# Kernel optimization log

Measured on AMD Instinct MI355X. Metric: run time of the kernel, lower is better.

Reference implementation:

```python
import jax, jax.numpy as jnp
import numpy as np

B, C, N, O, K = 4, 64, 8192, 128, 20


def setup_inputs() -> dict:
    key = jax.random.key(0)
    k1, k2, k3 = jax.random.split(key, 3)
    x = jax.random.normal(k1, (B, C, N), dtype=jnp.float32)
    # Conv2d(2C, 2C, 1, bias=False) weight squeezed to [2C, 2C]
    W1 = jax.random.normal(k2, (2 * C, 2 * C), dtype=jnp.float32) * (1.0 / np.sqrt(2 * C))
    # Conv2d(2C, O, 1, bias=False) weight squeezed to [O, 2C]
    W2 = jax.random.normal(k3, (O, 2 * C), dtype=jnp.float32) * (1.0 / np.sqrt(2 * C))
    return {"x": x, "W1": W1, "W2": W2, "spiral_size": K}


def _knn_idx(x, k):
    # x: [B, C, N]; negative squared pairwise distance, top-k = k nearest (incl. self)
    inner = -2.0 * jnp.einsum('bcn,bcm->bnm', x, x)          # [B, N, N]
    xx = jnp.sum(x * x, axis=1)                               # [B, N]
    pd = -xx[:, :, None] - inner - xx[:, None, :]             # [B, N, N]
    return jax.lax.top_k(pd, k)[1]                            # [B, N, k] int32


def reference(x, W1, W2, spiral_size):
    b, c, n = x.shape
    idx = _knn_idx(x, spiral_size)                            # [B, N, K]
    xt = jnp.transpose(x, (0, 2, 1))                          # [B, N, C]
    spirals = xt[jnp.arange(b)[:, None, None], idx]           # [B, N, K, C] neighbor gather
    center = jnp.broadcast_to(xt[:, :, None, :], spirals.shape)
    feats = jnp.concatenate([spirals - center, center], axis=-1)  # [B, N, K, 2C]
    h = jnp.einsum('bnkc,dc->bnkd', feats, W1)                # 1x1 conv1
    gate = jax.nn.softmax(h, axis=2)                          # softmax over neighbor dim K
    gated = feats * gate                                      # [B, N, K, 2C]
    out = jnp.einsum('bnkc,oc->bon', gated, W2)               # conv2 + sum over K -> [B, O, N]
    return out
```

## Files before the change

kernel.cpp:

```cpp
#include <hip/hip_runtime.h>
#include <math.h>

#define BB 4
#define CC 64
#define NN 8192
#define OO 128
#define KK 20
#define DD 128
#define NT 64
#define BUFSZ 10

typedef short bf16x8 __attribute__((ext_vector_type(8)));
typedef float f32x4 __attribute__((ext_vector_type(4)));
typedef unsigned short u16x8 __attribute__((ext_vector_type(8)));
typedef unsigned long long u64;

typedef __attribute__((address_space(1))) const void gvoid;
typedef __attribute__((address_space(3))) void lvoid;

__device__ __forceinline__ u64 packkey(float v, int idx) {
  unsigned u = __float_as_uint(v);
  unsigned o = ((int)u < 0) ? ~u : (u | 0x80000000u);
  return (((u64)o) << 32) | (unsigned)(~idx);
}
__device__ __forceinline__ float keyval(u64 k) {
  unsigned o = (unsigned)(k >> 32);
  unsigned u = (o & 0x80000000u) ? (o ^ 0x80000000u) : ~o;
  return __uint_as_float(u);
}
#define INITKEY (((u64)0x007FFFFFu) << 32)

__device__ __forceinline__ unsigned short bf_rne(float f) {
  unsigned u = __float_as_uint(f);
  u += 0x7FFFu + ((u >> 16) & 1u);
  return (unsigned short)(u >> 16);
}
__device__ __forceinline__ float bf_f(unsigned short h) {
  return __uint_as_float(((unsigned)h) << 16);
}

__global__ __launch_bounds__(128) void prep_kernel(const float* __restrict__ x,
                                                   float* __restrict__ xx,
                                                   unsigned short* __restrict__ xs) {
  const int tid = threadIdx.x;
  const int b = blockIdx.y;
  const int n0 = blockIdx.x * 128;
  const float* xb = x + (size_t)b * CC * NN;
  float xv[CC];
  float acc = 0.0f;
  #pragma unroll
  for (int c = 0; c < CC; ++c) {
    float v = xb[(size_t)c * NN + n0 + tid];
    acc += v * v;
    xv[c] = v;
  }
  xx[b * NN + n0 + tid] = acc;

  const int n = n0 + tid;
  char* xsrow = ((char*)xs) + ((size_t)b * NN + n) * 384;
  const int swn = (n & 7) << 4;
  #pragma unroll
  for (int gr = 0; gr < 8; ++gr) {
    u16x8 h8, m8, l8;
    #pragma unroll
    for (int e = 0; e < 8; ++e) {
      float v = xv[gr * 8 + e];
      unsigned short h = bf_rne(v);
      float r = v - bf_f(h);
      unsigned short m = bf_rne(r);
      r -= bf_f(m);
      unsigned short l = bf_rne(r);
      h8[e] = (unsigned short)h; m8[e] = m; l8[e] = l;
    }
    *(u16x8*)(xsrow + (((gr * 16) + 0) ^ swn)) = h8;
    *(u16x8*)(xsrow + (((gr * 16) + 128) ^ swn)) = m8;
    *(u16x8*)(xsrow + (((gr * 16) + 256) ^ swn)) = l8;
  }
}

__global__ __launch_bounds__(256, 4) void knn_kernel(
    const unsigned short* __restrict__ xs, const float* __restrict__ xx,
    u64* __restrict__ pkeys) {
  __shared__ __attribute__((aligned(16))) unsigned short atile[64 * 192];
  __shared__ float pdb[4][64][BUFSZ];
  __shared__ unsigned short idb[4][64][BUFSZ];
  __shared__ float cxx[64];
  const int tid = threadIdx.x;
  const int w = tid >> 6;
  const int lane = tid & 63;
  const int r = lane & 15;
  const int g = lane >> 4;
  const int lin = blockIdx.x;
  const int b = (lin & 7) >> 1;
  const int ch = lin & 1;
  const int qg = lin >> 3;
  const int qbase = qg * 64 + w * 16;
  const int q = qbase + r;
  const int cbase = ch * 4096;
  const char* xsb = ((const char*)xs) + (size_t)b * NN * 384;

  bf16x8 bq[3][2];
  {
    const char* qrow = xsb + (size_t)q * 384;
    const int sw = (q & 7) << 4;
    #pragma unroll
    for (int s = 0; s < 3; ++s)
      #pragma unroll
      for (int c = 0; c < 2; ++c)
        bq[s][c] = *(const bf16x8*)(qrow + ((s * 128 + c * 64 + g * 16) ^ sw));
  }
  const float xxq = xx[b * NN + q];

  u64 tk[KK];
  #pragma unroll
  for (int j = 0; j < KK; ++j) tk[j] = INITKEY;
  float minv = -INFINITY;
  int cnt = 0;
  float* pdl = &pdb[w][lane][0];
  unsigned short* idl = &idb[w][lane][0];

  auto stage = [&](int t) {
    const char* src = xsb + (size_t)(cbase + t * 64) * 384;
    char* dst = (char*)atile;
    #pragma unroll
    for (int it = 0; it < 6; ++it) {
      __builtin_amdgcn_global_load_lds(
          (gvoid*)(src + it * 4096 + tid * 16),
          (lvoid*)(dst + it * 4096 + tid * 16), 16, 0, 0);
    }
    if (tid < 16) {
      __builtin_amdgcn_global_load_lds(
          (gvoid*)(xx + b * NN + cbase + t * 64 + tid * 4),
          (lvoid*)(cxx + tid * 4), 16, 0, 0);
    }
  };

  auto rebuild = [&]() {
    int mxc = cnt;
    #pragma unroll
    for (int o = 32; o > 0; o >>= 1) {
      int v = __shfl_xor(mxc, o);
      mxc = mxc > v ? mxc : v;
    }
    for (int i = 0; i < mxc; ++i) {
      u64 k = (i < cnt) ? packkey(pdl[i], (int)idl[i]) : 0ULL;
      if (k > tk[KK - 1]) {
        #pragma unroll
        for (int jj = KK - 1; jj >= 1; --jj)
          tk[jj] = (k > tk[jj - 1]) ? tk[jj - 1] : ((k > tk[jj]) ? k : tk[jj]);
        tk[0] = (k > tk[0]) ? k : tk[0];
      }
    }
    cnt = 0;
    minv = keyval(tk[KK - 1]);
  };

  for (int t = 0; t < NT; ++t) {
    stage(t);
    __syncthreads();

    #pragma unroll
    for (int ct = 0; ct < 4; ++ct) {
      const char* arow = ((const char*)atile) + (ct * 16 + r) * 384;
      const int sw = (r & 7) << 4;
      bf16x8 a6[6];
      #pragma unroll
      for (int c6 = 0; c6 < 6; ++c6)
        a6[c6] = *(const bf16x8*)(arow + ((c6 * 64 + g * 16) ^ sw));
      f32x4 acc = {0.f, 0.f, 0.f, 0.f};
      __builtin_amdgcn_s_setprio(1);
      #pragma unroll
      for (int s = 2; s >= 0; --s)
        #pragma unroll
        for (int c6 = 0; c6 < 6; ++c6)
          acc = __builtin_amdgcn_mfma_f32_16x16x32_bf16(a6[c6], bq[s][c6 & 1],
                                                        acc, 0, 0, 0);
      __builtin_amdgcn_s_setprio(0);
      #pragma unroll
      for (int j = 0; j < 4; ++j) {
        const int ml = ct * 16 + g * 4 + j;
        float pd = (-xxq - (-2.0f * acc[j])) - cxx[ml];
        if (pd > minv) {
          pdl[cnt] = pd;
          idl[cnt] = (unsigned short)(cbase + t * 64 + ml);
          ++cnt;
        }
      }
      if (__any(cnt > 6)) rebuild();
    }
    __syncthreads();
  }

  rebuild();

  for (int pass = 0; pass < 2; ++pass) {
    if (pass) __syncthreads();
    if ((w >> 1) == pass) {
      u64* ml = ((u64*)atile) + (size_t)(w & 1) * 64 * KK;
      #pragma unroll
      for (int j = 0; j < KK; ++j) ml[lane * KK + j] = tk[j];
      if (lane < 16) {
        u64* po = pkeys + (((size_t)b * NN + qbase + lane) * 2 + ch) * KK;
        const u64* L0 = ml + (lane + 0) * KK;
        const u64* L1 = ml + (lane + 16) * KK;
        const u64* L2 = ml + (lane + 32) * KK;
        const u64* L3 = ml + (lane + 48) * KK;
        int p0 = 0, p1 = 0, p2 = 0, p3 = 0;
        u64 h0 = L0[0], h1 = L1[0], h2 = L2[0], h3 = L3[0];
        #pragma unroll
        for (int k = 0; k < KK; ++k) {
          u64 bv = h0; int bc = 0;
          if (h1 > bv) { bv = h1; bc = 1; }
          if (h2 > bv) { bv = h2; bc = 2; }
          if (h3 > bv) { bv = h3; bc = 3; }
          po[k] = bv;
          if (bc == 0)      { ++p0; h0 = (p0 < KK) ? L0[p0] : 0ULL; }
          else if (bc == 1) { ++p1; h1 = (p1 < KK) ? L1[p1] : 0ULL; }
          else if (bc == 2) { ++p2; h2 = (p2 < KK) ? L2[p2] : 0ULL; }
          else              { ++p3; h3 = (p3 < KK) ? L3[p3] : 0ULL; }
        }
      }
    }
  }
}

__global__ __launch_bounds__(256) void merge_kernel(const u64* __restrict__ pkeys,
                                                    int* __restrict__ fidx) {
  const int q = blockIdx.x * 256 + threadIdx.x;
  const u64* pk = pkeys + (size_t)q * 2 * KK;
  int* fo = fidx + (size_t)q * KK;
  int p0 = 0, p1 = 0;
  u64 h0 = pk[0], h1 = pk[KK];
  #pragma unroll
  for (int k = 0; k < KK; ++k) {
    const bool t1 = h1 > h0;
    const u64 bv = t1 ? h1 : h0;
    fo[k] = (int)(~(unsigned)bv);
    if (t1) { ++p1; h1 = (p1 < KK) ? pk[KK + p1] : 0ULL; }
    else    { ++p0; h0 = (p0 < KK) ? pk[p0] : 0ULL; }
  }
}

__global__ __launch_bounds__(256) void w1prep_kernel(const float* __restrict__ W1,
                                                     unsigned short* __restrict__ w1p) {
  for (int e = threadIdx.x; e < 12288; e += 256) {
    const int f = e >> 9;
    const int rr = e & 511;
    const int l = rr >> 3;
    const int j = rr & 7;
    const int pair = f / 3, s = f % 3;
    const int dt = pair >> 1, kc = pair & 1;
    const int d = dt * 16 + (l & 15);
    const int c = kc * 32 + (l >> 4) * 8 + j;
    const float v = W1[d * DD + c];
    const unsigned short h = bf_rne(v);
    float r = v - bf_f(h);
    const unsigned short m = bf_rne(r);
    r -= bf_f(m);
    const unsigned short lo = bf_rne(r);
    w1p[(size_t)f * 512 + l * 8 + j] = (s == 0) ? h : ((s == 1) ? m : lo);
  }
}

#define MFMA16(A, B, C) __builtin_amdgcn_mfma_f32_16x16x32_bf16((A), (B), (C), 0, 0, 0)

template <int SA, int SB>
__device__ __forceinline__ void h_term(const bf16x8 (&a)[3][2][2],
                                       const bf16x8 (&w1f)[24],
                                       f32x4 (&acc)[4][2]) {
  #pragma unroll
  for (int dt = 0; dt < 4; ++dt)
    #pragma unroll
    for (int kc = 0; kc < 2; ++kc) {
      const bf16x8 bf = w1f[(dt * 2 + kc) * 3 + SB];
      acc[dt][0] = MFMA16(a[SA][kc][0], bf, acc[dt][0]);
      acc[dt][1] = MFMA16(a[SA][kc][1], bf, acc[dt][1]);
    }
}

template <int DT>
__device__ __forceinline__ float d1_epi(const bf16x8 (&a)[3][2][2],
                                        bf16x8 id0, bf16x8 id1,
                                        const f32x4 (&acc)[4][2], int g) {
  constexpr int KC = DT >> 1;
  const bf16x8 idp = (DT & 1) ? id1 : id0;
  f32x4 yf0 = {0.f, 0.f, 0.f, 0.f}, yf1 = {0.f, 0.f, 0.f, 0.f};
  yf0 = MFMA16(a[1][KC][0], idp, yf0);
  yf0 = MFMA16(a[0][KC][0], idp, yf0);
  yf1 = MFMA16(a[1][KC][1], idp, yf1);
  yf1 = MFMA16(a[0][KC][1], idp, yf1);
  const f32x4 h0 = acc[DT][0], h1 = acc[DT][1];
  float mx = fmaxf(fmaxf(h0[0], h0[1]), fmaxf(h0[2], h0[3]));
  mx = fmaxf(mx, fmaxf(fmaxf(h1[0], h1[1]), fmaxf(h1[2], h1[3])));
  mx = fmaxf(mx, __shfl_xor(mx, 16));
  mx = fmaxf(mx, __shfl_xor(mx, 32));
  float sl = 0.f, tl = 0.f;
  #pragma unroll
  for (int j = 0; j < 4; ++j) {
    const float e = __expf(h0[j] - mx);
    sl += e; tl += yf0[j] * e;
  }
  if (g == 0) {
    #pragma unroll
    for (int j = 0; j < 4; ++j) {
      const float e = __expf(h1[j] - mx);
      sl += e; tl += yf1[j] * e;
    }
  }
  sl += __shfl_xor(sl, 16); sl += __shfl_xor(sl, 32);
  tl += __shfl_xor(tl, 16); tl += __shfl_xor(tl, 32);
  return tl / sl;
}

__global__ __launch_bounds__(256, 2) void d1_kernel(
    const unsigned short* __restrict__ xs, const int* __restrict__ fidx,
    const unsigned short* __restrict__ w1p, float* __restrict__ gbuf) {
  const int tid = threadIdx.x;
  const int w = tid >> 6;
  const int lane = tid & 63;
  const int r = lane & 15;
  const int g = lane >> 4;
  const int b = blockIdx.y;
  const char* xsb = ((const char*)xs) + (size_t)b * NN * 384;

  bf16x8 w1f[24];
  #pragma unroll
  for (int f = 0; f < 24; ++f)
    w1f[f] = *(const bf16x8*)(((const char*)w1p) + f * 1024 + lane * 16);

  bf16x8 id0, id1;
  #pragma unroll
  for (int j = 0; j < 8; ++j) {
    id0[j] = (g == (r >> 3) && j == (r & 7)) ? (short)0x3F80 : (short)0;
    id1[j] = (g == 2 + (r >> 3) && j == (r & 7)) ? (short)0x3F80 : (short)0;
  }

  for (int i = 0; i < 4; ++i) {
    const int n = blockIdx.x * 16 + w * 4 + i;
    const size_t ng = (size_t)b * NN + n;
    const int* kp = fidx + ng * KK;
    const int row0 = kp[r];
    const int row1 = kp[16 + (r & 3)];
    const char* rp0 = xsb + (size_t)row0 * 384;
    const char* rp1 = xsb + (size_t)row1 * 384;
    const int sw0 = (row0 & 7) << 4, sw1 = (row1 & 7) << 4;

    bf16x8 a[3][2][2];
    #pragma unroll
    for (int s = 0; s < 3; ++s)
      #pragma unroll
      for (int kc = 0; kc < 2; ++kc) {
        const int off = s * 128 + kc * 64 + g * 16;
        a[s][kc][0] = *(const bf16x8*)(rp0 + (off ^ sw0));
        a[s][kc][1] = *(const bf16x8*)(rp1 + (off ^ sw1));
      }

    const char* zrow = xsb + (size_t)n * 384;
    const int swn = (n & 7) << 4;
    float zl;
    {
      const unsigned short zh = *(const unsigned short*)(zrow + ((2 * lane) ^ swn));
      const unsigned short zm = *(const unsigned short*)(zrow + ((128 + 2 * lane) ^ swn));
      const unsigned short zo = *(const unsigned short*)(zrow + ((256 + 2 * lane) ^ swn));
      zl = bf_f(zh) + bf_f(zm) + bf_f(zo);
    }

    f32x4 acc[4][2];
    #pragma unroll
    for (int dt = 0; dt < 4; ++dt) {
      acc[dt][0] = (f32x4){0.f, 0.f, 0.f, 0.f};
      acc[dt][1] = (f32x4){0.f, 0.f, 0.f, 0.f};
    }
    h_term<2, 0>(a, w1f, acc);
    h_term<0, 2>(a, w1f, acc);
    h_term<1, 1>(a, w1f, acc);
    h_term<1, 0>(a, w1f, acc);
    h_term<0, 1>(a, w1f, acc);
    h_term<0, 0>(a, w1f, acc);

    const float t0 = d1_epi<0>(a, id0, id1, acc, g);
    const float t1 = d1_epi<1>(a, id0, id1, acc, g);
    const float t2 = d1_epi<2>(a, id0, id1, acc, g);
    const float t3 = d1_epi<3>(a, id0, id1, acc, g);

    float* go = gbuf + ng * DD;
    go[64 + lane] = zl;
    const float z0 = __shfl(zl, r);
    const float z1 = __shfl(zl, 16 + r);
    const float z2 = __shfl(zl, 32 + r);
    const float z3 = __shfl(zl, 48 + r);
    if (lane < 16) {
      go[r]      = t0 - z0;
      go[16 + r] = t1 - z1;
      go[32 + r] = t2 - z2;
      go[48 + r] = t3 - z3;
    }
  }
}

__global__ __launch_bounds__(256) void d2_kernel(const float* __restrict__ gbuf,
                                                 const float* __restrict__ W2,
                                                 float* __restrict__ out) {
  __shared__ float4 w2s[OO * 32];
  const int tid = threadIdx.x;
  const int b = blockIdx.y;
  const int n0 = blockIdx.x * 32;
  const float4* w2v = (const float4*)W2;
  for (int t = tid; t < OO * 32; t += 256) {
    int o = t >> 5, c4 = t & 31;
    w2s[o * 32 + (c4 ^ (o & 7))] = w2v[t];
  }
  __syncthreads();
  const int og = tid & 7;
  const int ni = tid >> 3;
  const int n = n0 + ni;
  const float4* gp = (const float4*)(gbuf + ((size_t)b * NN + n) * DD);
  float acc[16];
  #pragma unroll
  for (int j = 0; j < 16; ++j) acc[j] = 0.0f;
  for (int c4 = 0; c4 < 32; ++c4) {
    float4 g4 = gp[c4];
    #pragma unroll
    for (int j = 0; j < 16; ++j) {
      const int o = j * 8 + og;
      float4 w4 = w2s[o * 32 + (c4 ^ og)];
      acc[j] += g4.x * w4.x + g4.y * w4.y + g4.z * w4.z + g4.w * w4.w;
    }
  }
  float* outb = out + (size_t)b * OO * NN;
  #pragma unroll
  for (int j = 0; j < 16; ++j) {
    outb[(size_t)(j * 8 + og) * NN + n] = acc[j];
  }
}

extern "C" void kernel_launch(void* const* d_in, const int* in_sizes, int n_in,
                              void* d_out, int out_size, void* d_ws, size_t ws_size,
                              hipStream_t stream) {
  const float* x  = (const float*)d_in[0];
  const float* W1 = (const float*)d_in[1];
  const float* W2 = (const float*)d_in[2];
  float* out = (float*)d_out;
  char* ws = (char*)d_ws;
  unsigned short* xs = (unsigned short*)(ws);
  float* xx = (float*)(ws + 12582912);
  unsigned short* w1p = (unsigned short*)(ws + 12582912);
  int* fidx = (int*)(ws + 12713984);
  u64* pkeys = (u64*)(ws + 15335424);
  float* gbuf = (float*)(ws + 15335424);

  prep_kernel<<<dim3(NN / 128, BB), 128, 0, stream>>>(x, xx, xs);
  knn_kernel<<<dim3(1024), 256, 0, stream>>>(xs, xx, pkeys);
  merge_kernel<<<dim3(BB * NN / 256), 256, 0, stream>>>(pkeys, fidx);
  w1prep_kernel<<<dim3(1), 256, 0, stream>>>(W1, w1p);
  d1_kernel<<<dim3(NN / 16, BB), 256, 0, stream>>>(xs, fidx, w1p, gbuf);
  d2_kernel<<<dim3(NN / 32, BB), 256, 0, stream>>>(gbuf, W2, out);
}
```

Baseline: 708.3 us.

## Halve KNN candidate tile to raise occupancy and add wave-level skip of candidate insertion

Shrinks the per-iteration candidate tile from 64 to 32 points and the per-thread candidate buffer from 10 to 8 entries, which cuts LDS use so the launch bound can ask for 6 blocks per CU instead of 4. The candidate-filter step now computes all four distances first and skips the buffer-insert branch when no lane in the wave beats its current threshold. The merge scratch is split between the tile and buffer memory, since the tile alone is now too small for it. The cost is twice as many barrier and staging iterations, each carrying less MFMA work, and possible register pressure under the tighter launch bound.

```diff
diff --git a/kernel.cpp b/kernel.cpp
--- a/kernel.cpp
+++ b/kernel.cpp
@@ -7,8 +7,11 @@
 #define OO 128
 #define KK 20
 #define DD 128
-#define NT 64
-#define BUFSZ 10
+#define NCH 2
+#define CH (NN / NCH)
+#define TC 32
+#define NT (CH / TC)
+#define BUFSZ 8
 
 typedef short bf16x8 __attribute__((ext_vector_type(8)));
 typedef float f32x4 __attribute__((ext_vector_type(4)));
@@ -78,25 +81,28 @@
   }
 }
 
-__global__ __launch_bounds__(256, 4) void knn_kernel(
+__global__ __launch_bounds__(256, 6) void knn_kernel(
     const unsigned short* __restrict__ xs, const float* __restrict__ xx,
     u64* __restrict__ pkeys) {
-  __shared__ __attribute__((aligned(16))) unsigned short atile[64 * 192];
-  __shared__ float pdb[4][64][BUFSZ];
-  __shared__ unsigned short idb[4][64][BUFSZ];
-  __shared__ float cxx[64];
+  __shared__ __attribute__((aligned(16))) unsigned short atile[TC * 192];
+  __shared__ __attribute__((aligned(16))) char bufmem[4 * 64 * BUFSZ * 6];
+  __shared__ float cxx[TC];
+  float* pdb = (float*)bufmem;
+  unsigned short* idb = (unsigned short*)(bufmem + 4 * 64 * BUFSZ * 4);
+
   const int tid = threadIdx.x;
   const int w = tid >> 6;
   const int lane = tid & 63;
   const int r = lane & 15;
   const int g = lane >> 4;
   const int lin = blockIdx.x;
-  const int b = (lin & 7) >> 1;
-  const int ch = lin & 1;
+  const int xcd = lin & 7;
+  const int b = xcd >> 1;
+  const int ch = xcd & 1;
   const int qg = lin >> 3;
   const int qbase = qg * 64 + w * 16;
   const int q = qbase + r;
-  const int cbase = ch * 4096;
+  const int cbase = ch * CH;
   const char* xsb = ((const char*)xs) + (size_t)b * NN * 384;
 
   bf16x8 bq[3][2];
@@ -116,23 +122,22 @@
   for (int j = 0; j < KK; ++j) tk[j] = INITKEY;
   float minv = -INFINITY;
   int cnt = 0;
-  float* pdl = &pdb[w][lane][0];
-  unsigned short* idl = &idb[w][lane][0];
+  float* pdl = pdb + (w * 64 + lane) * BUFSZ;
+  unsigned short* idl = idb + (w * 64 + lane) * BUFSZ;
 
   auto stage = [&](int t) {
-    const char* src = xsb + (size_t)(cbase + t * 64) * 384;
+    const char* src = xsb + (size_t)(cbase + t * TC) * 384;
     char* dst = (char*)atile;
     #pragma unroll
-    for (int it = 0; it < 6; ++it) {
+    for (int it = 0; it < 3; ++it) {
       __builtin_amdgcn_global_load_lds(
           (gvoid*)(src + it * 4096 + tid * 16),
           (lvoid*)(dst + it * 4096 + tid * 16), 16, 0, 0);
     }
-    if (tid < 16) {
+    if (tid < 8)
       __builtin_amdgcn_global_load_lds(
-          (gvoid*)(xx + b * NN + cbase + t * 64 + tid * 4),
+          (gvoid*)(xx + b * NN + cbase + t * TC + tid * 4),
           (lvoid*)(cxx + tid * 4), 16, 0, 0);
-    }
   };
 
   auto rebuild = [&]() {
@@ -160,7 +165,7 @@
     __syncthreads();
 
     #pragma unroll
-    for (int ct = 0; ct < 4; ++ct) {
+    for (int ct = 0; ct < 2; ++ct) {
       const char* arow = ((const char*)atile) + (ct * 16 + r) * 384;
       const int sw = (r & 7) << 4;
       bf16x8 a6[6];
@@ -176,17 +181,20 @@
           acc = __builtin_amdgcn_mfma_f32_16x16x32_bf16(a6[c6], bq[s][c6 & 1],
                                                         acc, 0, 0, 0);
       __builtin_amdgcn_s_setprio(0);
-      #pragma unroll
-      for (int j = 0; j < 4; ++j) {
-        const int ml = ct * 16 + g * 4 + j;
-        float pd = (-xxq - (-2.0f * acc[j])) - cxx[ml];
-        if (pd > minv) {
-          pdl[cnt] = pd;
-          idl[cnt] = (unsigned short)(cbase + t * 64 + ml);
-          ++cnt;
-        }
+
+      float pd0 = (-xxq - (-2.0f * acc[0])) - cxx[ct * 16 + g * 4 + 0];
+      float pd1 = (-xxq - (-2.0f * acc[1])) - cxx[ct * 16 + g * 4 + 1];
+      float pd2 = (-xxq - (-2.0f * acc[2])) - cxx[ct * 16 + g * 4 + 2];
+      float pd3 = (-xxq - (-2.0f * acc[3])) - cxx[ct * 16 + g * 4 + 3];
+      const float maxpd = fmaxf(fmaxf(pd0, pd1), fmaxf(pd2, pd3));
+      if (__any(maxpd > minv)) {
+        const int i0 = cbase + t * TC + ct * 16 + g * 4;
+        if (pd0 > minv) { pdl[cnt] = pd0; idl[cnt] = (unsigned short)(i0 + 0); ++cnt; }
+        if (pd1 > minv) { pdl[cnt] = pd1; idl[cnt] = (unsigned short)(i0 + 1); ++cnt; }
+        if (pd2 > minv) { pdl[cnt] = pd2; idl[cnt] = (unsigned short)(i0 + 2); ++cnt; }
+        if (pd3 > minv) { pdl[cnt] = pd3; idl[cnt] = (unsigned short)(i0 + 3); ++cnt; }
+        if (__any(cnt > BUFSZ - 4)) rebuild();
       }
-      if (__any(cnt > 6)) rebuild();
     }
     __syncthreads();
   }
@@ -194,13 +202,13 @@
   rebuild();
 
   for (int pass = 0; pass < 2; ++pass) {
-    if (pass) __syncthreads();
+    __syncthreads();
     if ((w >> 1) == pass) {
-      u64* ml = ((u64*)atile) + (size_t)(w & 1) * 64 * KK;
+      u64* ml = (w & 1) ? (u64*)bufmem : (u64*)atile;
       #pragma unroll
       for (int j = 0; j < KK; ++j) ml[lane * KK + j] = tk[j];
       if (lane < 16) {
-        u64* po = pkeys + (((size_t)b * NN + qbase + lane) * 2 + ch) * KK;
+        u64* po = pkeys + (((size_t)b * NN + qbase + lane) * NCH + ch) * KK;
         const u64* L0 = ml + (lane + 0) * KK;
         const u64* L1 = ml + (lane + 16) * KK;
         const u64* L2 = ml + (lane + 32) * KK;
@@ -227,7 +235,7 @@
 __global__ __launch_bounds__(256) void merge_kernel(const u64* __restrict__ pkeys,
                                                     int* __restrict__ fidx) {
   const int q = blockIdx.x * 256 + threadIdx.x;
-  const u64* pk = pkeys + (size_t)q * 2 * KK;
+  const u64* pk = pkeys + (size_t)q * NCH * KK;
   int* fo = fidx + (size_t)q * KK;
   int p0 = 0, p1 = 0;
   u64 h0 = pk[0], h1 = pk[KK];
```

Measured after the change: 2.052 ms. 190% more time.
